# Performance work log

Hardware: AMD Instinct MI355X
Metric: run time of the kernel (lower is better)

The kernel has to match this reference:

```python
import jax, jax.numpy as jnp
import numpy as np

N = 16384          # batch of signals
DIM_T = 256        # time steps per signal
DT = 0.01          # integration dt (intg_lev=1 -> dt_intg = dt)
NUF = 256          # num_units_feat
HID_XI = 128       # hidlayers_xi
HID_AUX = 64       # hidlayers_aux1_dec
LEN_INTG = DIM_T   # (dim_t-1)*intg_lev + 1 with intg_lev=1


def _linear_init(key, fan_in, fan_out):
    # torch nn.Linear default: U(-1/sqrt(fan_in), 1/sqrt(fan_in))
    s = 1.0 / np.sqrt(fan_in)
    kw, kb = jax.random.split(key)
    W = jax.random.uniform(kw, (fan_in, fan_out), minval=-s, maxval=s, dtype=jnp.float32)
    b = jax.random.uniform(kb, (fan_out,), minval=-s, maxval=s, dtype=jnp.float32)
    return W, b


def setup_inputs() -> dict:
    key = jax.random.key(0)
    ks = jax.random.split(key, 12)
    data = jax.random.normal(ks[0], (N, DIM_T), dtype=jnp.float32)
    omega = jax.random.normal(ks[1], (N, 1), dtype=jnp.float32)
    eps = jax.random.normal(ks[2], (N, 1), dtype=jnp.float32)
    # feature extractor (mlp branch): [dim_t+1 -> 256 -> 256], relu after both (actfun_output=True)
    W_feat1, b_feat1 = _linear_init(ks[3], DIM_T + 1, NUF)
    W_feat2, b_feat2 = _linear_init(ks[4], NUF, NUF)
    # xi mean head: MLP [256 -> 128 -> 1] then Softplus
    W_xim1, b_xim1 = _linear_init(ks[5], NUF, HID_XI)
    W_xim2, b_xim2 = _linear_init(ks[6], HID_XI, 1)
    # xi lnvar head: MLP [256 -> 128 -> 1]
    W_xil1, b_xil1 = _linear_init(ks[7], NUF, HID_XI)
    W_xil2, b_xil2 = _linear_init(ks[8], HID_XI, 1)
    # decoder aux1 MLP: [dim_z_aux1+1=2 -> 64 -> 1]
    W_aux1, b_aux1 = _linear_init(ks[9], 2, HID_AUX)
    W_aux2, b_aux2 = _linear_init(ks[10], HID_AUX, 1)
    return dict(data=data, omega=omega, eps=eps,
                W_feat1=W_feat1, b_feat1=b_feat1, W_feat2=W_feat2, b_feat2=b_feat2,
                W_xim1=W_xim1, b_xim1=b_xim1, W_xim2=W_xim2, b_xim2=b_xim2,
                W_xil1=W_xil1, b_xil1=b_xil1, W_xil2=W_xil2, b_xil2=b_xil2,
                W_aux1=W_aux1, b_aux1=b_aux1, W_aux2=W_aux2, b_aux2=b_aux2)


def reference(data, omega, eps,
              W_feat1, b_feat1, W_feat2, b_feat2,
              W_xim1, b_xim1, W_xim2, b_xim2,
              W_xil1, b_xil1, W_xil2, b_xil2,
              W_aux1, b_aux1, W_aux2, b_aux2):
    relu = jax.nn.relu
    # ---- encode_xi ----
    x_ = jnp.concatenate([data, omega], axis=1)                 # [n, dim_t+1]
    feat = relu(relu(x_ @ W_feat1 + b_feat1) @ W_feat2 + b_feat2)  # [n, 256]
    xi_mean = jax.nn.softplus(relu(feat @ W_xim1 + b_xim1) @ W_xim2 + b_xim2)  # [n, 1]
    xi_lnvar = relu(feat @ W_xil1 + b_xil1) @ W_xil2 + b_xil2                  # [n, 1]
    # ---- draw (reparameterization + clamp to feasible range [0, 1]) ----
    xi = xi_mean + jnp.exp(0.5 * xi_lnvar) * eps
    xi = jnp.clip(xi, 0.0, 1.0)
    # ---- decode: Euler odeint over LEN_INTG steps of state yy=[y, dy/dt] ----
    init_y = data[:, :1]                                        # [n, 1]
    initcond = jnp.concatenate([init_y, jnp.zeros_like(init_y)], axis=1)  # [n, 2]

    def step(yy, _):
        # physics: d[y, v]/dt = [v, 0]; aux MLP adds acceleration from (z_aux1=omega, y)
        aux_in = jnp.concatenate([omega, yy[:, :1]], axis=1)    # [n, 2]
        acc = relu(aux_in @ W_aux1 + b_aux1) @ W_aux2 + b_aux2  # [n, 1]
        dyy = jnp.concatenate([yy[:, 1:2], acc], axis=1)        # [n, 2]
        return yy + DT * dyy, yy

    _, yy_seq = jax.lax.scan(step, initcond, None, length=LEN_INTG)  # [len_intg, n, 2]
    y_seq = yy_seq[:, :, 0].T                                   # [n, dim_t] (intg_lev=1)
    t_intg = DT * jnp.arange(LEN_INTG, dtype=jnp.float32)       # [dim_t]
    x_PAB = jnp.exp(-jnp.abs(xi) * t_intg[None, :]) * y_seq     # [n, dim_t]
    return xi_mean, xi_lnvar, x_PAB
```

## Files before the change

### kernel.cpp

```cpp
#include <hip/hip_runtime.h>
#include <math.h>

#define NROWS 16384
#define DT_C 0.01f

typedef short s16x8 __attribute__((ext_vector_type(8)));
typedef float f32x4 __attribute__((ext_vector_type(4)));
typedef float f32x2 __attribute__((ext_vector_type(2)));

__device__ __forceinline__ unsigned short f2bf(float f) {
    unsigned u = __float_as_uint(f);
    u += 0x7fffu + ((u >> 16) & 1u);
    return (unsigned short)(u >> 16);
}
__device__ __forceinline__ unsigned pack2bf(float a, float b) {
    return (unsigned)f2bf(a) | ((unsigned)f2bf(b) << 16);
}
template <int CTRL>
__device__ __forceinline__ float dppadd(float v) {
    int x = __builtin_amdgcn_update_dpp(0, __float_as_int(v), CTRL, 0xF, 0xF, true);
    return v + __int_as_float(x);
}
__device__ __forceinline__ float sum8(float p) {
    p = dppadd<0xB1>(p);
    p = dppadd<0x4E>(p);
    p = dppadd<0x141>(p);
    return p;
}

__global__ __launch_bounds__(256) void prep_k(
    const float* __restrict__ Wf1, const float* __restrict__ Wf2,
    const float* __restrict__ Wm1, const float* __restrict__ Wl1,
    const float* __restrict__ bm1, const float* __restrict__ bl1,
    unsigned short* __restrict__ wpack, float* __restrict__ biasH)
{
    const int id = blockIdx.x * 256 + threadIdx.x;
    const int n  = id & 255;
    const int k8 = (id >> 8) & 31;
    const int s  = id >> 13;

    unsigned short tmp[8];
    #pragma unroll
    for (int j = 0; j < 8; ++j) {
        const int k = k8 * 8 + j;
        float v;
        if (s == 0)      v = Wf1[k * 256 + n];
        else if (s == 1) v = Wf2[k * 256 + n];
        else             v = (n < 128) ? Wm1[k * 128 + n] : Wl1[k * 128 + n - 128];
        tmp[j] = f2bf(v);
    }
    *(uint4*)&wpack[((s * 32 + k8) * 256 + n) * 8] = *(const uint4*)tmp;

    if (id < 256) biasH[id] = (id < 128) ? bm1[id] : bl1[id - 128];
}

__global__ __launch_bounds__(256, 2) void fused_k(
    const float* __restrict__ data, const float* __restrict__ omega,
    const float* __restrict__ eps_g,
    const unsigned short* __restrict__ wpack, const float* __restrict__ biasH,
    const float* __restrict__ bf1, const float* __restrict__ bf2,
    const float* __restrict__ w256g,
    const float* __restrict__ Wm2, const float* __restrict__ bm2,
    const float* __restrict__ Wl2, const float* __restrict__ bl2,
    const float* __restrict__ Wa1, const float* __restrict__ ba1,
    const float* __restrict__ Wa2, const float* __restrict__ ba2,
    float* __restrict__ out_mean, float* __restrict__ out_lnvar,
    float* __restrict__ xout)
{
    __shared__ __align__(16) unsigned char smem[33024];
    unsigned short* As1 = (unsigned short*)smem;
    unsigned short* Hs  = (unsigned short*)(smem + 16384);
    float* headsF = (float*)smem;
    float* omg = (float*)(smem + 32768);
    float* xiS = omg + 32;

    const int tid  = threadIdx.x;
    const int wid  = tid >> 6;
    const int lane = tid & 63;
    const int ln   = lane & 15;
    const int quad = lane >> 4;
    const int r0   = blockIdx.x * 32;

    {
        #pragma unroll
        for (int g2 = 0; g2 < 8; ++g2) {
            const int unit = g2 * 256 + tid;
            const int m    = unit >> 6;
            const int c16  = unit & 63;
            const int kblk = c16 >> 1;
            const int h    = c16 & 1;
            const float4 v = *(const float4*)&data[(size_t)(r0 + m) * 256 + c16 * 4];
            unsigned* d = (unsigned*)&As1[((kblk * 32) + (m ^ (kblk & 7))) * 8 + h * 4];
            d[0] = pack2bf(v.x, v.y);
            d[1] = pack2bf(v.z, v.w);
        }
        if (tid < 32) omg[tid] = omega[r0 + tid];
    }
    __syncthreads();

    {
        const int r   = tid >> 3;
        const int l   = tid & 7;
        const int row = r0 + r;
        const float om = omg[r];
        const float pseed = ba2[0] * 0.125f;

        f32x2 w1v[4], Av[4], w2v[4];
        #pragma unroll
        for (int i = 0; i < 4; ++i) {
            const f32x2 w0 = *(const f32x2*)&Wa1[l * 8 + i * 2];
            const f32x2 bb = *(const f32x2*)&ba1[l * 8 + i * 2];
            w1v[i] = *(const f32x2*)&Wa1[64 + l * 8 + i * 2];
            w2v[i] = *(const f32x2*)&Wa2[l * 8 + i * 2];
            Av[i]  = f32x2{fmaf(om, w0.x, bb.x), fmaf(om, w0.y, bb.y)};
        }

        auto partial = [&](float y) -> float {
            const f32x2 y2 = f32x2{y, y};
            f32x2 acc2 = f32x2{pseed, 0.f};
            #pragma unroll
            for (int i = 0; i < 4; ++i) {
                f32x2 h = __builtin_elementwise_fma(y2, w1v[i], Av[i]);
                h = __builtin_elementwise_max(h, f32x2{0.f, 0.f});
                acc2 = __builtin_elementwise_fma(h, w2v[i], acc2);
            }
            return acc2.x + acc2.y;
        };

        const float y0 = data[(size_t)row * 256];
        float ym = y0;
        float yc = y0;
        const float DT2 = DT_C * DT_C;
        float pr = sum8(partial(ym));

        float* orow = xout + (size_t)row * 256 + l * 4;
        for (int tb = 0; tb < 8; ++tb) {
            float cur[4];
            #pragma unroll
            for (int j = 0; j < 32; ++j) {
                if ((j >> 2) == l) cur[j & 3] = ym;
                float pn = sum8(partial(yc));
                const float ynext = fmaf(DT2, pr, fmaf(2.f, yc, -ym));
                ym = yc; yc = ynext; pr = pn;
            }
            *(float4*)&orow[tb * 32] = *(const float4*)cur;
        }
    }

    f32x4 acc[2][4];

    auto seed = [&](const float* bias) {
        #pragma unroll
        for (int nt = 0; nt < 4; ++nt) {
            const float b = bias[wid * 64 + nt * 16 + ln];
            acc[0][nt] = f32x4{b, b, b, b};
            acc[1][nt] = acc[0][nt];
        }
    };

    auto run_stage = [&](const unsigned short* Ap, const unsigned short* wp) {
        #pragma unroll
        for (int c = 0; c < 4; ++c) {
            #pragma unroll
            for (int kk = 0; kk < 2; ++kk) {
                const int kb   = kk * 4 + quad;
                const int kblk = c * 8 + kb;
                const int f    = kblk & 7;
                s16x8 b0 = *(const s16x8*)&wp[((size_t)(kblk * 256) + wid * 64 + 0 * 16 + ln) * 8];
                s16x8 b1 = *(const s16x8*)&wp[((size_t)(kblk * 256) + wid * 64 + 1 * 16 + ln) * 8];
                s16x8 b2 = *(const s16x8*)&wp[((size_t)(kblk * 256) + wid * 64 + 2 * 16 + ln) * 8];
                s16x8 b3 = *(const s16x8*)&wp[((size_t)(kblk * 256) + wid * 64 + 3 * 16 + ln) * 8];
                s16x8 a0 = *(const s16x8*)&Ap[(kblk * 32 + (ln ^ f)) * 8];
                s16x8 a1 = *(const s16x8*)&Ap[(kblk * 32 + ((ln ^ f) + 16)) * 8];
                acc[0][0] = __builtin_amdgcn_mfma_f32_16x16x32_bf16(a0, b0, acc[0][0], 0, 0, 0);
                acc[1][0] = __builtin_amdgcn_mfma_f32_16x16x32_bf16(a1, b0, acc[1][0], 0, 0, 0);
                acc[0][1] = __builtin_amdgcn_mfma_f32_16x16x32_bf16(a0, b1, acc[0][1], 0, 0, 0);
                acc[1][1] = __builtin_amdgcn_mfma_f32_16x16x32_bf16(a1, b1, acc[1][1], 0, 0, 0);
                acc[0][2] = __builtin_amdgcn_mfma_f32_16x16x32_bf16(a0, b2, acc[0][2], 0, 0, 0);
                acc[1][2] = __builtin_amdgcn_mfma_f32_16x16x32_bf16(a1, b2, acc[1][2], 0, 0, 0);
                acc[0][3] = __builtin_amdgcn_mfma_f32_16x16x32_bf16(a0, b3, acc[0][3], 0, 0, 0);
                acc[1][3] = __builtin_amdgcn_mfma_f32_16x16x32_bf16(a1, b3, acc[1][3], 0, 0, 0);
            }
        }
    };

    auto write_packed = [&](unsigned short* dst, bool addOm) {
        #pragma unroll
        for (int nt = 0; nt < 4; ++nt) {
            const int col = wid * 64 + nt * 16 + ln;
            const int kg  = col >> 3, f = kg & 7, jj = col & 7;
            const float wo = addOm ? w256g[col] : 0.f;
            #pragma unroll
            for (int mt = 0; mt < 2; ++mt) {
                #pragma unroll
                for (int r = 0; r < 4; ++r) {
                    const int row = mt * 16 + quad * 4 + r;
                    float v = acc[mt][nt][r];
                    if (addOm) v = fmaf(omg[row], wo, v);
                    v = fmaxf(v, 0.f);
                    dst[(kg * 32 + (row ^ f)) * 8 + jj] = f2bf(v);
                }
            }
        }
    };

    seed(bf1);
    run_stage(As1, wpack);
    write_packed(Hs, true);
    __syncthreads();
    seed(bf2);
    run_stage(Hs, wpack + 65536);
    write_packed(As1, false);
    __syncthreads();
    seed(biasH);
    run_stage(As1, wpack + 131072);
    __syncthreads();
    #pragma unroll
    for (int nt = 0; nt < 4; ++nt) {
        const int col = wid * 64 + nt * 16 + ln;
        #pragma unroll
        for (int mt = 0; mt < 2; ++mt) {
            #pragma unroll
            for (int r = 0; r < 4; ++r) {
                const int row = mt * 16 + quad * 4 + r;
                headsF[row * 256 + ((col + row * 8) & 255)] = fmaxf(acc[mt][nt][r], 0.f);
            }
        }
    }
    __syncthreads();

    {
        const int m = tid >> 3, l = tid & 7;
        float pm = 0.f, pl = 0.f;
        #pragma unroll
        for (int q = 0; q < 4; ++q) {
            const int c0 = l * 16 + q * 4;
            const float4 hm = *(const float4*)&headsF[m * 256 + ((c0 + m * 8) & 255)];
            const float4 wm = *(const float4*)&Wm2[c0];
            const float4 hl = *(const float4*)&headsF[m * 256 + ((128 + c0 + m * 8) & 255)];
            const float4 wl = *(const float4*)&Wl2[c0];
            pm = fmaf(hm.w, wm.w, fmaf(hm.z, wm.z, fmaf(hm.y, wm.y, fmaf(hm.x, wm.x, pm))));
            pl = fmaf(hl.w, wl.w, fmaf(hl.z, wl.z, fmaf(hl.y, wl.y, fmaf(hl.x, wl.x, pl))));
        }
        pm = sum8(pm);
        pl = sum8(pl);
        if (l == 0) {
            const float xm  = pm + bm2[0];
            const float mean = fmaxf(xm, 0.f) + log1pf(expf(-fabsf(xm)));
            const float lnv  = pl + bl2[0];
            out_mean[r0 + m]  = mean;
            out_lnvar[r0 + m] = lnv;
            float xi = mean + expf(0.5f * lnv) * eps_g[r0 + m];
            xiS[m] = fminf(fmaxf(xi, 0.f), 1.f);
        }
    }
    __syncthreads();

    {
        const int r   = tid >> 3;
        const int l   = tid & 7;
        const float nxdt = -xiS[r] * DT_C;
        float* orow = xout + (size_t)(r0 + r) * 256 + l * 4;
        #pragma unroll
        for (int tb = 0; tb < 8; ++tb) {
            float4 v = *(const float4*)&orow[tb * 32];
            const int c0 = tb * 32 + l * 4;
            v.x *= __expf(nxdt * (float)(c0 + 0));
            v.y *= __expf(nxdt * (float)(c0 + 1));
            v.z *= __expf(nxdt * (float)(c0 + 2));
            v.w *= __expf(nxdt * (float)(c0 + 3));
            *(float4*)&orow[tb * 32] = v;
        }
    }
}

extern "C" void kernel_launch(void* const* d_in, const int* in_sizes, int n_in,
                              void* d_out, int out_size, void* d_ws, size_t ws_size,
                              hipStream_t stream)
{
    const float* data    = (const float*)d_in[0];
    const float* omega   = (const float*)d_in[1];
    const float* eps     = (const float*)d_in[2];
    const float* W_feat1 = (const float*)d_in[3];
    const float* b_feat1 = (const float*)d_in[4];
    const float* W_feat2 = (const float*)d_in[5];
    const float* b_feat2 = (const float*)d_in[6];
    const float* W_xim1  = (const float*)d_in[7];
    const float* b_xim1  = (const float*)d_in[8];
    const float* W_xim2  = (const float*)d_in[9];
    const float* b_xim2  = (const float*)d_in[10];
    const float* W_xil1  = (const float*)d_in[11];
    const float* b_xil1  = (const float*)d_in[12];
    const float* W_xil2  = (const float*)d_in[13];
    const float* b_xil2  = (const float*)d_in[14];
    const float* W_aux1  = (const float*)d_in[15];
    const float* b_aux1  = (const float*)d_in[16];
    const float* W_aux2  = (const float*)d_in[17];
    const float* b_aux2  = (const float*)d_in[18];

    float* out_mean  = (float*)d_out;
    float* out_lnvar = out_mean + NROWS;
    float* out_x     = out_lnvar + NROWS;

    unsigned short* wpack = (unsigned short*)d_ws;
    float* biasH = (float*)((char*)d_ws + 3 * 32 * 256 * 8 * 2);

    prep_k<<<96, 256, 0, stream>>>(W_feat1, W_feat2, W_xim1, W_xil1,
                                   b_xim1, b_xil1, wpack, biasH);
    fused_k<<<512, 256, 0, stream>>>(data, omega, eps, wpack, biasH,
                                     b_feat1, b_feat2, W_feat1 + 256 * 256,
                                     W_xim2, b_xim2, W_xil2, b_xil2,
                                     W_aux1, b_aux1, W_aux2, b_aux2,
                                     out_mean, out_lnvar, out_x);
}
```

Before: 139.9 us.

## Split ODE integration into separate kernel with 4 lanes per row and fused decay

Moves the Euler ODE integration out of the fused MLP kernel into a second kernel. That kernel uses 4 lanes per row instead of 8, so each lane evaluates 16 hidden units and the cross-lane reduction takes two DPP steps instead of three. The exponential decay is folded in as a running product of exp(-xi*dt), which removes the global write-read-write pass over the output. The cost is an extra kernel launch, an xi round trip through workspace memory, fewer rows per block in the ODE grid, and a small numerical drift from the repeated multiplication.

Measured after the change: 141.1 us. No clear change (+0.9%).

```diff
diff --git a/kernel.cpp b/kernel.cpp
--- a/kernel.cpp
+++ b/kernel.cpp
@@ -20,6 +20,11 @@
 __device__ __forceinline__ float dppadd(float v) {
     int x = __builtin_amdgcn_update_dpp(0, __float_as_int(v), CTRL, 0xF, 0xF, true);
     return v + __int_as_float(x);
+}
+__device__ __forceinline__ float sum4(float p) {
+    p = dppadd<0xB1>(p);
+    p = dppadd<0x4E>(p);
+    return p;
 }
 __device__ __forceinline__ float sum8(float p) {
     p = dppadd<0xB1>(p);
@@ -54,7 +59,7 @@
     if (id < 256) biasH[id] = (id < 128) ? bm1[id] : bl1[id - 128];
 }
 
-__global__ __launch_bounds__(256, 2) void fused_k(
+__global__ __launch_bounds__(256, 2) void mega_k(
     const float* __restrict__ data, const float* __restrict__ omega,
     const float* __restrict__ eps_g,
     const unsigned short* __restrict__ wpack, const float* __restrict__ biasH,
@@ -62,17 +67,14 @@
     const float* __restrict__ w256g,
     const float* __restrict__ Wm2, const float* __restrict__ bm2,
     const float* __restrict__ Wl2, const float* __restrict__ bl2,
-    const float* __restrict__ Wa1, const float* __restrict__ ba1,
-    const float* __restrict__ Wa2, const float* __restrict__ ba2,
     float* __restrict__ out_mean, float* __restrict__ out_lnvar,
-    float* __restrict__ xout)
+    float* __restrict__ xi_ws)
 {
-    __shared__ __align__(16) unsigned char smem[33024];
+    __shared__ __align__(16) unsigned char smem[32896];
     unsigned short* As1 = (unsigned short*)smem;
     unsigned short* Hs  = (unsigned short*)(smem + 16384);
     float* headsF = (float*)smem;
     float* omg = (float*)(smem + 32768);
-    float* xiS = omg + 32;
 
     const int tid  = threadIdx.x;
     const int wid  = tid >> 6;
@@ -95,56 +97,6 @@
             d[1] = pack2bf(v.z, v.w);
         }
         if (tid < 32) omg[tid] = omega[r0 + tid];
-    }
-    __syncthreads();
-
-    {
-        const int r   = tid >> 3;
-        const int l   = tid & 7;
-        const int row = r0 + r;
-        const float om = omg[r];
-        const float pseed = ba2[0] * 0.125f;
-
-        f32x2 w1v[4], Av[4], w2v[4];
-        #pragma unroll
-        for (int i = 0; i < 4; ++i) {
-            const f32x2 w0 = *(const f32x2*)&Wa1[l * 8 + i * 2];
-            const f32x2 bb = *(const f32x2*)&ba1[l * 8 + i * 2];
-            w1v[i] = *(const f32x2*)&Wa1[64 + l * 8 + i * 2];
-            w2v[i] = *(const f32x2*)&Wa2[l * 8 + i * 2];
-            Av[i]  = f32x2{fmaf(om, w0.x, bb.x), fmaf(om, w0.y, bb.y)};
-        }
-
-        auto partial = [&](float y) -> float {
-            const f32x2 y2 = f32x2{y, y};
-            f32x2 acc2 = f32x2{pseed, 0.f};
-            #pragma unroll
-            for (int i = 0; i < 4; ++i) {
-                f32x2 h = __builtin_elementwise_fma(y2, w1v[i], Av[i]);
-                h = __builtin_elementwise_max(h, f32x2{0.f, 0.f});
-                acc2 = __builtin_elementwise_fma(h, w2v[i], acc2);
-            }
-            return acc2.x + acc2.y;
-        };
-
-        const float y0 = data[(size_t)row * 256];
-        float ym = y0;
-        float yc = y0;
-        const float DT2 = DT_C * DT_C;
-        float pr = sum8(partial(ym));
-
-        float* orow = xout + (size_t)row * 256 + l * 4;
-        for (int tb = 0; tb < 8; ++tb) {
-            float cur[4];
-            #pragma unroll
-            for (int j = 0; j < 32; ++j) {
-                if ((j >> 2) == l) cur[j & 3] = ym;
-                float pn = sum8(partial(yc));
-                const float ynext = fmaf(DT2, pr, fmaf(2.f, yc, -ym));
-                ym = yc; yc = ynext; pr = pn;
-            }
-            *(float4*)&orow[tb * 32] = *(const float4*)cur;
-        }
     }
 
     f32x4 acc[2][4];
@@ -204,6 +156,7 @@
         }
     };
 
+    __syncthreads();
     seed(bf1);
     run_stage(As1, wpack);
     write_packed(Hs, true);
@@ -245,32 +198,86 @@
         pm = sum8(pm);
         pl = sum8(pl);
         if (l == 0) {
-            const float xm  = pm + bm2[0];
+            const float xm   = pm + bm2[0];
             const float mean = fmaxf(xm, 0.f) + log1pf(expf(-fabsf(xm)));
             const float lnv  = pl + bl2[0];
             out_mean[r0 + m]  = mean;
             out_lnvar[r0 + m] = lnv;
             float xi = mean + expf(0.5f * lnv) * eps_g[r0 + m];
-            xiS[m] = fminf(fmaxf(xi, 0.f), 1.f);
-        }
-    }
-    __syncthreads();
-
-    {
-        const int r   = tid >> 3;
-        const int l   = tid & 7;
-        const float nxdt = -xiS[r] * DT_C;
-        float* orow = xout + (size_t)(r0 + r) * 256 + l * 4;
-        #pragma unroll
-        for (int tb = 0; tb < 8; ++tb) {
-            float4 v = *(const float4*)&orow[tb * 32];
-            const int c0 = tb * 32 + l * 4;
-            v.x *= __expf(nxdt * (float)(c0 + 0));
-            v.y *= __expf(nxdt * (float)(c0 + 1));
-            v.z *= __expf(nxdt * (float)(c0 + 2));
-            v.w *= __expf(nxdt * (float)(c0 + 3));
-            *(float4*)&orow[tb * 32] = v;
-        }
+            xi_ws[r0 + m] = fminf(fmaxf(xi, 0.f), 1.f);
+        }
+    }
+}
+
+__global__ __launch_bounds__(256) void ode2_k(
+    const float* __restrict__ data, const float* __restrict__ omega_g,
+    const float* __restrict__ xi_ws,
+    const float* __restrict__ Wa1, const float* __restrict__ ba1,
+    const float* __restrict__ Wa2, const float* __restrict__ ba2,
+    float* __restrict__ xout)
+{
+    const int tid = threadIdx.x;
+    const int r   = tid >> 2;
+    const int l   = tid & 3;
+    const int row = blockIdx.x * 64 + r;
+
+    const float om = omega_g[row];
+    const float xi = xi_ws[row];
+    const float s  = expf(-xi * DT_C);
+    const float pseed = ba2[0] * 0.25f;
+
+    f32x2 w1v[8], Av[8], w2v[8];
+    #pragma unroll
+    for (int i = 0; i < 8; ++i) {
+        const int u = l * 16 + i * 2;
+        const f32x2 w0 = *(const f32x2*)&Wa1[u];
+        const f32x2 bb = *(const f32x2*)&ba1[u];
+        w1v[i] = *(const f32x2*)&Wa1[64 + u];
+        w2v[i] = *(const f32x2*)&Wa2[u];
+        Av[i]  = f32x2{fmaf(om, w0.x, bb.x), fmaf(om, w0.y, bb.y)};
+    }
+
+    auto partial = [&](float y) -> float {
+        const f32x2 y2 = f32x2{y, y};
+        f32x2 a0 = f32x2{pseed, 0.f};
+        f32x2 a1 = f32x2{0.f, 0.f};
+        f32x2 a2 = f32x2{0.f, 0.f};
+        f32x2 a3 = f32x2{0.f, 0.f};
+        #pragma unroll
+        for (int i = 0; i < 8; ++i) {
+            f32x2 h = __builtin_elementwise_fma(y2, w1v[i], Av[i]);
+            h = __builtin_elementwise_max(h, f32x2{0.f, 0.f});
+            if ((i & 3) == 0) a0 = __builtin_elementwise_fma(h, w2v[i], a0);
+            if ((i & 3) == 1) a1 = __builtin_elementwise_fma(h, w2v[i], a1);
+            if ((i & 3) == 2) a2 = __builtin_elementwise_fma(h, w2v[i], a2);
+            if ((i & 3) == 3) a3 = __builtin_elementwise_fma(h, w2v[i], a3);
+        }
+        a0 = a0 + a1;
+        a2 = a2 + a3;
+        a0 = a0 + a2;
+        return a0.x + a0.y;
+    };
+
+    const float y0 = data[(size_t)row * 256];
+    float ym = y0;
+    float yc = y0;
+    const float DT2 = DT_C * DT_C;
+    float pr = sum4(partial(ym));
+    float d = 1.f;
+
+    float* orow = xout + (size_t)row * 256 + l * 4;
+    for (int b = 0; b < 16; ++b) {
+        float cur[4] = {0.f, 0.f, 0.f, 0.f};
+        #pragma unroll
+        for (int j = 0; j < 16; ++j) {
+            const float m_ = d * ym;
+            if ((j >> 2) == l) cur[j & 3] = m_;
+            d *= s;
+            float pn = sum4(partial(yc));
+            const float ynext = fmaf(DT2, pr, fmaf(2.f, yc, -ym));
+            ym = yc; yc = ynext; pr = pn;
+        }
+        *(float4*)&orow[b * 16] = *(const float4*)cur;
     }
 }
 
@@ -304,12 +311,14 @@
 
     unsigned short* wpack = (unsigned short*)d_ws;
     float* biasH = (float*)((char*)d_ws + 3 * 32 * 256 * 8 * 2);
+    float* xi_ws = biasH + 256;
 
     prep_k<<<96, 256, 0, stream>>>(W_feat1, W_feat2, W_xim1, W_xil1,
                                    b_xim1, b_xil1, wpack, biasH);
-    fused_k<<<512, 256, 0, stream>>>(data, omega, eps, wpack, biasH,
-                                     b_feat1, b_feat2, W_feat1 + 256 * 256,
-                                     W_xim2, b_xim2, W_xil2, b_xil2,
-                                     W_aux1, b_aux1, W_aux2, b_aux2,
-                                     out_mean, out_lnvar, out_x);
-}
+    mega_k<<<512, 256, 0, stream>>>(data, omega, eps, wpack, biasH,
+                                    b_feat1, b_feat2, W_feat1 + 256 * 256,
+                                    W_xim2, b_xim2, W_xil2, b_xil2,
+                                    out_mean, out_lnvar, xi_ws);
+    ode2_k<<<256, 256, 0, stream>>>(data, omega, xi_ws,
+                                    W_aux1, b_aux1, W_aux2, b_aux2, out_x);
+}
```

## Fuse decay multiply into ODE integration and move integration after heads

Applied to the files above, without the earlier changes.

Moves the Euler ODE integration to after the xi computation so the exponential decay can be applied inline with a running product, instead of writing y_seq to global memory and then re-reading and rescaling it. Also replaces round-to-nearest bf16 conversion with truncation (byte perm / shift), simplifies B-fragment address arithmetic, and splits the aux-MLP accumulation into two chains for more ILP. Truncation slightly changes numerics, and the cumulative-product decay can drift from exp(-xi*t) over 256 steps.

Measured after the change: 142.9 us. 2.2% more time.

```diff
diff --git a/kernel.cpp b/kernel.cpp
--- a/kernel.cpp
+++ b/kernel.cpp
@@ -13,8 +13,8 @@
     u += 0x7fffu + ((u >> 16) & 1u);
     return (unsigned short)(u >> 16);
 }
-__device__ __forceinline__ unsigned pack2bf(float a, float b) {
-    return (unsigned)f2bf(a) | ((unsigned)f2bf(b) << 16);
+__device__ __forceinline__ unsigned packtr(float a, float b) {
+    return __builtin_amdgcn_perm(__float_as_uint(b), __float_as_uint(a), 0x07060302u);
 }
 template <int CTRL>
 __device__ __forceinline__ float dppadd(float v) {
@@ -91,60 +91,10 @@
             const int h    = c16 & 1;
             const float4 v = *(const float4*)&data[(size_t)(r0 + m) * 256 + c16 * 4];
             unsigned* d = (unsigned*)&As1[((kblk * 32) + (m ^ (kblk & 7))) * 8 + h * 4];
-            d[0] = pack2bf(v.x, v.y);
-            d[1] = pack2bf(v.z, v.w);
+            d[0] = packtr(v.x, v.y);
+            d[1] = packtr(v.z, v.w);
         }
         if (tid < 32) omg[tid] = omega[r0 + tid];
-    }
-    __syncthreads();
-
-    {
-        const int r   = tid >> 3;
-        const int l   = tid & 7;
-        const int row = r0 + r;
-        const float om = omg[r];
-        const float pseed = ba2[0] * 0.125f;
-
-        f32x2 w1v[4], Av[4], w2v[4];
-        #pragma unroll
-        for (int i = 0; i < 4; ++i) {
-            const f32x2 w0 = *(const f32x2*)&Wa1[l * 8 + i * 2];
-            const f32x2 bb = *(const f32x2*)&ba1[l * 8 + i * 2];
-            w1v[i] = *(const f32x2*)&Wa1[64 + l * 8 + i * 2];
-            w2v[i] = *(const f32x2*)&Wa2[l * 8 + i * 2];
-            Av[i]  = f32x2{fmaf(om, w0.x, bb.x), fmaf(om, w0.y, bb.y)};
-        }
-
-        auto partial = [&](float y) -> float {
-            const f32x2 y2 = f32x2{y, y};
-            f32x2 acc2 = f32x2{pseed, 0.f};
-            #pragma unroll
-            for (int i = 0; i < 4; ++i) {
-                f32x2 h = __builtin_elementwise_fma(y2, w1v[i], Av[i]);
-                h = __builtin_elementwise_max(h, f32x2{0.f, 0.f});
-                acc2 = __builtin_elementwise_fma(h, w2v[i], acc2);
-            }
-            return acc2.x + acc2.y;
-        };
-
-        const float y0 = data[(size_t)row * 256];
-        float ym = y0;
-        float yc = y0;
-        const float DT2 = DT_C * DT_C;
-        float pr = sum8(partial(ym));
-
-        float* orow = xout + (size_t)row * 256 + l * 4;
-        for (int tb = 0; tb < 8; ++tb) {
-            float cur[4];
-            #pragma unroll
-            for (int j = 0; j < 32; ++j) {
-                if ((j >> 2) == l) cur[j & 3] = ym;
-                float pn = sum8(partial(yc));
-                const float ynext = fmaf(DT2, pr, fmaf(2.f, yc, -ym));
-                ym = yc; yc = ynext; pr = pn;
-            }
-            *(float4*)&orow[tb * 32] = *(const float4*)cur;
-        }
     }
 
     f32x4 acc[2][4];
@@ -166,10 +116,11 @@
                 const int kb   = kk * 4 + quad;
                 const int kblk = c * 8 + kb;
                 const int f    = kblk & 7;
-                s16x8 b0 = *(const s16x8*)&wp[((size_t)(kblk * 256) + wid * 64 + 0 * 16 + ln) * 8];
-                s16x8 b1 = *(const s16x8*)&wp[((size_t)(kblk * 256) + wid * 64 + 1 * 16 + ln) * 8];
-                s16x8 b2 = *(const s16x8*)&wp[((size_t)(kblk * 256) + wid * 64 + 2 * 16 + ln) * 8];
-                s16x8 b3 = *(const s16x8*)&wp[((size_t)(kblk * 256) + wid * 64 + 3 * 16 + ln) * 8];
+                const unsigned short* bp = wp + ((size_t)(kblk * 256) + wid * 64 + ln) * 8;
+                s16x8 b0 = *(const s16x8*)(bp + 0 * 128);
+                s16x8 b1 = *(const s16x8*)(bp + 1 * 128);
+                s16x8 b2 = *(const s16x8*)(bp + 2 * 128);
+                s16x8 b3 = *(const s16x8*)(bp + 3 * 128);
                 s16x8 a0 = *(const s16x8*)&Ap[(kblk * 32 + (ln ^ f)) * 8];
                 s16x8 a1 = *(const s16x8*)&Ap[(kblk * 32 + ((ln ^ f) + 16)) * 8];
                 acc[0][0] = __builtin_amdgcn_mfma_f32_16x16x32_bf16(a0, b0, acc[0][0], 0, 0, 0);
@@ -198,12 +149,14 @@
                     float v = acc[mt][nt][r];
                     if (addOm) v = fmaf(omg[row], wo, v);
                     v = fmaxf(v, 0.f);
-                    dst[(kg * 32 + (row ^ f)) * 8 + jj] = f2bf(v);
+                    dst[(kg * 32 + (row ^ f)) * 8 + jj] =
+                        (unsigned short)(__float_as_uint(v) >> 16);
                 }
             }
         }
     };
 
+    __syncthreads();
     seed(bf1);
     run_stage(As1, wpack);
     write_packed(Hs, true);
@@ -245,7 +198,7 @@
         pm = sum8(pm);
         pl = sum8(pl);
         if (l == 0) {
-            const float xm  = pm + bm2[0];
+            const float xm   = pm + bm2[0];
             const float mean = fmaxf(xm, 0.f) + log1pf(expf(-fabsf(xm)));
             const float lnv  = pl + bl2[0];
             out_mean[r0 + m]  = mean;
@@ -259,17 +212,55 @@
     {
         const int r   = tid >> 3;
         const int l   = tid & 7;
-        const float nxdt = -xiS[r] * DT_C;
-        float* orow = xout + (size_t)(r0 + r) * 256 + l * 4;
-        #pragma unroll
+        const int row = r0 + r;
+        const float om = omg[r];
+        const float s  = __expf(-xiS[r] * DT_C);
+        const float pseed = ba2[0] * 0.125f;
+
+        f32x2 w1v[4], Av[4], w2v[4];
+        #pragma unroll
+        for (int i = 0; i < 4; ++i) {
+            const f32x2 w0 = *(const f32x2*)&Wa1[l * 8 + i * 2];
+            const f32x2 bb = *(const f32x2*)&ba1[l * 8 + i * 2];
+            w1v[i] = *(const f32x2*)&Wa1[64 + l * 8 + i * 2];
+            w2v[i] = *(const f32x2*)&Wa2[l * 8 + i * 2];
+            Av[i]  = f32x2{fmaf(om, w0.x, bb.x), fmaf(om, w0.y, bb.y)};
+        }
+
+        auto partial = [&](float y) -> float {
+            const f32x2 y2 = f32x2{y, y};
+            f32x2 a0 = f32x2{pseed, 0.f};
+            f32x2 a1 = f32x2{0.f, 0.f};
+            #pragma unroll
+            for (int i = 0; i < 4; ++i) {
+                f32x2 h = __builtin_elementwise_fma(y2, w1v[i], Av[i]);
+                h = __builtin_elementwise_max(h, f32x2{0.f, 0.f});
+                if (i & 1) a1 = __builtin_elementwise_fma(h, w2v[i], a1);
+                else       a0 = __builtin_elementwise_fma(h, w2v[i], a0);
+            }
+            a0 = a0 + a1;
+            return a0.x + a0.y;
+        };
+
+        const float y0 = data[(size_t)row * 256];
+        float ym = y0, yc = y0;
+        const float DT2 = DT_C * DT_C;
+        float pr = sum8(partial(ym));
+        float d = 1.f;
+
+        float* orow = xout + (size_t)row * 256 + l * 4;
         for (int tb = 0; tb < 8; ++tb) {
-            float4 v = *(const float4*)&orow[tb * 32];
-            const int c0 = tb * 32 + l * 4;
-            v.x *= __expf(nxdt * (float)(c0 + 0));
-            v.y *= __expf(nxdt * (float)(c0 + 1));
-            v.z *= __expf(nxdt * (float)(c0 + 2));
-            v.w *= __expf(nxdt * (float)(c0 + 3));
-            *(float4*)&orow[tb * 32] = v;
+            float cur[4];
+            #pragma unroll
+            for (int j = 0; j < 32; ++j) {
+                const float m_ = d * ym;
+                if ((j >> 2) == l) cur[j & 3] = m_;
+                d *= s;
+                float pn = sum8(partial(yc));
+                const float yn = fmaf(DT2, pr, fmaf(2.f, yc, -ym));
+                ym = yc; yc = yn; pr = pn;
+            }
+            *(float4*)&orow[tb * 32] = *(const float4*)cur;
         }
     }
 }
```
